# Kernel tuning notes

Measured on AMD Instinct MI355X. Metric: run time of the kernel, lower is better.

Reference implementation:

```python
import jax, jax.numpy as jnp
import numpy as np

EMBED, HEADS, LEVELS, POINTS = 256, 8, 3, 4
SPATIAL = np.array([[128, 128], [64, 64], [32, 32]], dtype=np.int64)  # (H, W) per level
B = 2
S = int((SPATIAL[:, 0] * SPATIAL[:, 1]).sum())  # 21504
Q = S  # encoder self-attention: queries == flattened multi-scale features


def grid_sample_bilinear(img, grid):
    """img: [N,C,H,W]; grid: [N,Q,P,2] (x,y) in [-1,1]; bilinear, zeros padding, align_corners=False.
    Returns [N,C,Q,P]."""
    N, C, H, W = img.shape
    _, Qn, Pn, _ = grid.shape
    x = (grid[..., 0] + 1.0) * (W * 0.5) - 0.5
    y = (grid[..., 1] + 1.0) * (H * 0.5) - 0.5
    x0 = jnp.floor(x)
    y0 = jnp.floor(y)
    wx1 = x - x0
    wy1 = y - y0
    x0i = x0.astype(jnp.int32)
    y0i = y0.astype(jnp.int32)
    imgf = img.reshape(N, C, H * W)

    def gather(ix, iy):
        valid = (ix >= 0) & (ix < W) & (iy >= 0) & (iy < H)
        ixc = jnp.clip(ix, 0, W - 1)
        iyc = jnp.clip(iy, 0, H - 1)
        flat = (iyc * W + ixc).reshape(N, -1)  # [N, Q*P]
        v = jax.vmap(lambda im, f: im[:, f])(imgf, flat)  # [N, C, Q*P]
        return jnp.where(valid.reshape(N, 1, -1), v, 0.0)

    w00 = ((1.0 - wx1) * (1.0 - wy1)).reshape(N, 1, -1)
    w01 = (wx1 * (1.0 - wy1)).reshape(N, 1, -1)
    w10 = ((1.0 - wx1) * wy1).reshape(N, 1, -1)
    w11 = (wx1 * wy1).reshape(N, 1, -1)
    out = (gather(x0i, y0i) * w00 + gather(x0i + 1, y0i) * w01
           + gather(x0i, y0i + 1) * w10 + gather(x0i + 1, y0i + 1) * w11)
    return out.reshape(N, C, Qn, Pn)


def msda_forward(hidden_states, encoder_hidden_states, reference_points, shapes_np,
                 sampling_offsets_w, sampling_offsets_b, attention_weights_w, attention_weights_b,
                 value_proj_w, value_proj_b, output_proj_w, output_proj_b):
    Bn, Qn, E = hidden_states.shape
    H, L, P = HEADS, LEVELS, POINTS
    D = E // H
    Sn = encoder_hidden_states.shape[1]
    value = (encoder_hidden_states @ value_proj_w.T + value_proj_b).reshape(Bn, Sn, H, D)
    off = (hidden_states @ sampling_offsets_w.T + sampling_offsets_b).reshape(Bn, Qn, H, L, P, 2)
    aw = hidden_states @ attention_weights_w.T + attention_weights_b
    aw = jax.nn.softmax(aw.reshape(Bn, Qn, H, L * P), axis=-1).reshape(Bn, Qn, H, L, P)
    # offset normalizer is (W, H) per level
    norm = jnp.asarray(np.stack([shapes_np[:, 1], shapes_np[:, 0]], axis=-1), dtype=hidden_states.dtype)
    loc = reference_points[:, :, None, :, None, :] + off / norm[None, None, None, :, None, :]
    grids = 2.0 * loc - 1.0  # [B,Q,H,L,P,2]
    out = jnp.zeros((Bn * H, D, Qn), value.dtype)
    start = 0
    for lvl in range(L):  # small static loop over levels (distinct spatial shapes)
        h, w = int(shapes_np[lvl, 0]), int(shapes_np[lvl, 1])
        val_l = value[:, start:start + h * w].transpose(0, 2, 3, 1).reshape(Bn * H, D, h, w)
        start += h * w
        g = grids[:, :, :, lvl].transpose(0, 2, 1, 3, 4).reshape(Bn * H, Qn, P, 2)
        sampled = grid_sample_bilinear(val_l, g)  # [B*H, D, Q, P]
        w_l = aw[:, :, :, lvl].transpose(0, 2, 1, 3).reshape(Bn * H, 1, Qn, P)
        out = out + (sampled * w_l).sum(-1)
    out = out.reshape(Bn, H * D, Qn).transpose(0, 2, 1)  # [B,Q,E]
    return out @ output_proj_w.T + output_proj_b


def setup_inputs():
    key = jax.random.key(0)
    ks = jax.random.split(key, 11)
    sc = 0.02
    E, H, L, P = EMBED, HEADS, LEVELS, POINTS
    return {
        "hidden_states": jax.random.normal(ks[0], (B, Q, E), jnp.float32),
        "encoder_hidden_states": jax.random.normal(ks[1], (B, S, E), jnp.float32),
        "reference_points": jax.random.uniform(ks[2], (B, Q, L, 2), jnp.float32),
        "spatial_shapes": jnp.asarray(SPATIAL),
        "sampling_offsets_w": jax.random.normal(ks[3], (H * L * P * 2, E), jnp.float32) * sc,
        "sampling_offsets_b": jax.random.normal(ks[4], (H * L * P * 2,), jnp.float32) * sc,
        "attention_weights_w": jax.random.normal(ks[5], (H * L * P, E), jnp.float32) * sc,
        "attention_weights_b": jax.random.normal(ks[6], (H * L * P,), jnp.float32) * sc,
        "value_proj_w": jax.random.normal(ks[7], (E, E), jnp.float32) * sc,
        "value_proj_b": jax.random.normal(ks[8], (E,), jnp.float32) * sc,
        "output_proj_w": jax.random.normal(ks[9], (E, E), jnp.float32) * sc,
        "output_proj_b": jax.random.normal(ks[10], (E,), jnp.float32) * sc,
    }


def reference(hidden_states, encoder_hidden_states, reference_points, spatial_shapes,
              sampling_offsets_w, sampling_offsets_b, attention_weights_w, attention_weights_b,
              value_proj_w, value_proj_b, output_proj_w, output_proj_b):
    shapes_np = np.asarray(spatial_shapes)  # static per-level (H, W)
    return msda_forward(hidden_states, encoder_hidden_states, reference_points, shapes_np,
                        sampling_offsets_w, sampling_offsets_b, attention_weights_w, attention_weights_b,
                        value_proj_w, value_proj_b, output_proj_w, output_proj_b)
```

## Files before the change

### kernel.cpp

```cpp
#include <hip/hip_runtime.h>
#include <hip/hip_bf16.h>

#define EMBED   256
#define HEADS   8
#define LEVELS  3
#define POINTS  4
#define BATCH   2
#define QLEN    21504
#define SLEN    21504
#define MTOT    (BATCH * QLEN)

typedef __attribute__((ext_vector_type(8))) short short8;
typedef __attribute__((ext_vector_type(4))) float f32x4;

__device__ __forceinline__ short f2bf(float x) {
    unsigned u = __builtin_bit_cast(unsigned, x);
    u += 0x7fffu + ((u >> 16) & 1u);
    return (short)(u >> 16);
}
__device__ __forceinline__ float bf_lo(unsigned u) { return __builtin_bit_cast(float, u << 16); }
__device__ __forceinline__ float bf_hi(unsigned u) { return __builtin_bit_cast(float, u & 0xffff0000u); }
__device__ __forceinline__ void async16(const void* g, void* l) {
    __builtin_amdgcn_global_load_lds((const __attribute__((address_space(1))) void*)g,
                                     (__attribute__((address_space(3))) void*)l, 16, 0, 0);
}

__global__ __launch_bounds__(256)
void pack_weights_kernel(const float* __restrict__ vW, const float* __restrict__ oW,
                         const float* __restrict__ soW, const float* __restrict__ awW,
                         const float* __restrict__ soB, const float* __restrict__ awB,
                         short* __restrict__ vWb, short* __restrict__ oWb,
                         short* __restrict__ soawWb, float* __restrict__ soawB)
{
    int i = blockIdx.x * 256 + threadIdx.x;
    if (i < 65536) {
        vWb[i] = f2bf(vW[i]);
    } else if (i < 131072) {
        int j = i - 65536;
        oWb[j] = f2bf(oW[j]);
    } else if (i < 229376) {
        int j = i - 131072;
        int row = j >> 8, k = j & 255;
        float v = (row < 192) ? soW[row * 256 + k]
                 : (row < 288) ? awW[(row - 192) * 256 + k] : 0.f;
        soawWb[j] = f2bf(v);
    } else if (i < 229760) {
        int row = i - 229376;
        soawB[row] = (row < 192) ? soB[row] : (row < 288) ? awB[row - 192] : 0.f;
    }
}

template<bool A_FP32, bool OUT_BF16>
__device__ __forceinline__
void stream_gemm(const void* __restrict__ Aptr, const short* __restrict__ Wt,
                 const float* __restrict__ bias, void* __restrict__ Cout,
                 int ldc, int colbase, int rowstrip, short* __restrict__ Ws)
{
    const int tid  = threadIdx.x;
    const int lane = tid & 63;
    const int wv   = tid >> 6;
    const int m16  = lane & 15;
    const int ko   = lane >> 4;

    #pragma unroll
    for (int i = 0; i < 16; ++i) {
        const int c    = i * 256 + tid;
        const int colL = c >> 5;
        const int cw   = c & 31;
        const int csw  = (cw & 24) | ((cw ^ colL) & 7);
        async16(Wt + (((size_t)(colbase + colL)) << 8) + csw * 8, Ws + c * 8);
    }

    const int row = rowstrip + wv * 16 + m16;
    short8 afr[8];
    if (A_FP32) {
        const float* Af = (const float*)Aptr + (size_t)row * 256 + ko * 8;
        #pragma unroll
        for (int kt = 0; kt < 8; ++kt) {
            float4 x = *(const float4*)(Af + kt * 32);
            float4 y = *(const float4*)(Af + kt * 32 + 4);
            short8 t;
            t[0] = f2bf(x.x); t[1] = f2bf(x.y); t[2] = f2bf(x.z); t[3] = f2bf(x.w);
            t[4] = f2bf(y.x); t[5] = f2bf(y.y); t[6] = f2bf(y.z); t[7] = f2bf(y.w);
            afr[kt] = t;
        }
    } else {
        const short* Ab = (const short*)Aptr + (size_t)row * 256 + ko * 8;
        #pragma unroll
        for (int kt = 0; kt < 8; ++kt) afr[kt] = *(const short8*)(Ab + kt * 32);
    }

    __syncthreads();

    const short8* Wvp = (const short8*)Ws;
    const int r0 = rowstrip + wv * 16 + ko * 4;
    #pragma unroll
    for (int ct = 0; ct < 8; ++ct) {
        const int colL = ct * 16 + m16;
        const int rowc = colL * 32;
        f32x4 a = (f32x4)0.f;
        #pragma unroll
        for (int kt = 0; kt < 8; ++kt) {
            const int g = kt * 4 + ko;
            const int s = (g & 24) | ((g ^ colL) & 7);
            a = __builtin_amdgcn_mfma_f32_16x16x32_bf16(afr[kt], Wvp[rowc + s], a, 0, 0, 0);
        }
        const int col = colbase + colL;
        const float bv = bias[col];
        #pragma unroll
        for (int r = 0; r < 4; ++r) {
            const float v = a[r] + bv;
            if (OUT_BF16) ((short*)Cout)[(size_t)(r0 + r) * ldc + col] = f2bf(v);
            else          ((float*)Cout)[(size_t)(r0 + r) * ldc + col] = v;
        }
    }
}

__global__ __launch_bounds__(256)
void proj_gemm_kernel(const float* __restrict__ enc, const short* __restrict__ vWb,
                      const float* __restrict__ vB, short* __restrict__ valb,
                      const float* __restrict__ hs, const short* __restrict__ soawWb,
                      const float* __restrict__ soawB, float* __restrict__ offaw)
{
    __shared__ short Ws[128 * 256];
    const int rowstrip = blockIdx.y * 64;
    if (blockIdx.x < 2) {
        stream_gemm<true, true>(enc, vWb, vB, valb, 256, blockIdx.x * 128, rowstrip, Ws);
    } else {
        stream_gemm<true, false>(hs, soawWb, soawB, offaw, 384, (blockIdx.x - 2) * 128, rowstrip, Ws);
    }
}

__global__ __launch_bounds__(256)
void out_gemm_kernel(const short* __restrict__ A, const short* __restrict__ oWb,
                     const float* __restrict__ oB, float* __restrict__ C)
{
    __shared__ short Ws[128 * 256];
    stream_gemm<false, false>(A, oWb, oB, C, 256, blockIdx.x * 128, blockIdx.y * 64, Ws);
}

__global__ __launch_bounds__(256)
void msda_sample_kernel(const short* __restrict__ value,
                        const float* __restrict__ offaw,
                        const float* __restrict__ ref,
                        short* __restrict__ attn)
{
    __shared__ int prep[64 * 100];

    const int tid = threadIdx.x;
    const int g   = tid >> 2;
    const int sub = tid & 3;
    const int lq  = g >> 3;
    const int h   = g & 7;
    const int bq  = blockIdx.x * 8 + lq;
    const int b   = bq / QLEN;

    {
        const float* awp = offaw + (size_t)bq * 384 + 192 + h * 12;
        float w[12];
        #pragma unroll
        for (int i = 0; i < 12; ++i) w[i] = awp[i];
        float mx = w[0];
        #pragma unroll
        for (int i = 1; i < 12; ++i) mx = fmaxf(mx, w[i]);
        float s = 0.f;
        #pragma unroll
        for (int i = 0; i < 12; ++i) s += __expf(w[i] - mx);
        const float inv = 1.f / s;

        const float* offp = offaw + (size_t)bq * 384 + h * 24;
        const float* refp = ref + (size_t)bq * 6;

        #pragma unroll
        for (int it = 0; it < 3; ++it) {
            const int p  = sub + it * 4;
            const int l  = p >> 2;
            const int Wl = 128 >> l;
            const int st = (l == 0) ? 0 : (l == 1 ? 16384 : 20480);

            const float ox = offp[p * 2 + 0];
            const float oy = offp[p * 2 + 1];
            const float rx = refp[2 * l + 0];
            const float ry = refp[2 * l + 1];
            const float a  = __expf(w[p] - mx) * inv;

            const float x = fmaf(rx, (float)Wl, ox - 0.5f);
            const float y = fmaf(ry, (float)Wl, oy - 0.5f);
            const float x0f = floorf(x), y0f = floorf(y);
            const int   x0  = (int)x0f,  y0  = (int)y0f;
            const float wx1 = x - x0f, wy1 = y - y0f;
            const float wx0 = 1.f - wx1, wy0 = 1.f - wy1;
            const bool vx0 = (unsigned)x0       < (unsigned)Wl;
            const bool vx1 = (unsigned)(x0 + 1) < (unsigned)Wl;
            const bool vy0 = (unsigned)y0       < (unsigned)Wl;
            const bool vy1 = (unsigned)(y0 + 1) < (unsigned)Wl;

            const int r0c = (b * SLEN + st + y0 * Wl + x0) * 32 + h * 4;
            int4 idx; float4 wvv;
            idx.x = (vy0 && vx0) ? r0c                : 0;
            idx.y = (vy0 && vx1) ? r0c + 32           : 0;
            idx.z = (vy1 && vx0) ? r0c + Wl * 32      : 0;
            idx.w = (vy1 && vx1) ? r0c + Wl * 32 + 32 : 0;
            wvv.x = (vy0 && vx0) ? wy0 * wx0 * a : 0.f;
            wvv.y = (vy0 && vx1) ? wy0 * wx1 * a : 0.f;
            wvv.z = (vy1 && vx0) ? wy1 * wx0 * a : 0.f;
            wvv.w = (vy1 && vx1) ? wy1 * wx1 * a : 0.f;

            *(int4*)  &prep[g * 100 + p * 8]     = idx;
            *(float4*)&prep[g * 100 + p * 8 + 4] = wvv;
        }
    }
    __syncthreads();

    const int4* vp = (const int4*)value;
    float acc[8];
    #pragma unroll
    for (int j = 0; j < 8; ++j) acc[j] = 0.f;

    #pragma unroll
    for (int p = 0; p < 12; ++p) {
        const int4   idx = *(const int4*)  &prep[g * 100 + p * 8];
        const float4 wvv = *(const float4*)&prep[g * 100 + p * 8 + 4];
        const int4 v0 = vp[idx.x + sub];
        const int4 v1 = vp[idx.y + sub];
        const int4 v2 = vp[idx.z + sub];
        const int4 v3 = vp[idx.w + sub];
        #define ACCUM(V, W) \
            acc[0] = fmaf(W, bf_lo((unsigned)V.x), acc[0]); \
            acc[1] = fmaf(W, bf_hi((unsigned)V.x), acc[1]); \
            acc[2] = fmaf(W, bf_lo((unsigned)V.y), acc[2]); \
            acc[3] = fmaf(W, bf_hi((unsigned)V.y), acc[3]); \
            acc[4] = fmaf(W, bf_lo((unsigned)V.z), acc[4]); \
            acc[5] = fmaf(W, bf_hi((unsigned)V.z), acc[5]); \
            acc[6] = fmaf(W, bf_lo((unsigned)V.w), acc[6]); \
            acc[7] = fmaf(W, bf_hi((unsigned)V.w), acc[7]);
        ACCUM(v0, wvv.x) ACCUM(v1, wvv.y) ACCUM(v2, wvv.z) ACCUM(v3, wvv.w)
        #undef ACCUM
    }

    int4 o;
    o.x = ((unsigned)(unsigned short)f2bf(acc[1]) << 16) | (unsigned short)f2bf(acc[0]);
    o.y = ((unsigned)(unsigned short)f2bf(acc[3]) << 16) | (unsigned short)f2bf(acc[2]);
    o.z = ((unsigned)(unsigned short)f2bf(acc[5]) << 16) | (unsigned short)f2bf(acc[4]);
    o.w = ((unsigned)(unsigned short)f2bf(acc[7]) << 16) | (unsigned short)f2bf(acc[6]);
    ((int4*)attn)[(size_t)bq * 32 + h * 4 + sub] = o;
}

extern "C" void kernel_launch(void* const* d_in, const int* in_sizes, int n_in,
                              void* d_out, int out_size, void* d_ws, size_t ws_size,
                              hipStream_t stream) {
    const float* hs  = (const float*)d_in[0];
    const float* enc = (const float*)d_in[1];
    const float* rp  = (const float*)d_in[2];
    const float* soW = (const float*)d_in[4];
    const float* soB = (const float*)d_in[5];
    const float* awW = (const float*)d_in[6];
    const float* awB = (const float*)d_in[7];
    const float* vW  = (const float*)d_in[8];
    const float* vB  = (const float*)d_in[9];
    const float* oW  = (const float*)d_in[10];
    const float* oB  = (const float*)d_in[11];
    float* out = (float*)d_out;

    const int M = MTOT;
    const size_t ME = (size_t)M * 256;

    short* valb   = (short*)d_ws;
    short* attnb  = valb + ME;
    float* offaw  = (float*)(attnb + ME);
    short* vWb    = (short*)(offaw + (size_t)M * 384);
    short* oWb    = vWb + 65536;
    short* soawWb = oWb + 65536;
    float* soawB  = (float*)(soawWb + 98304);

    dim3 blk(256);
    pack_weights_kernel<<<dim3(898), blk, 0, stream>>>(vW, oW, soW, awW, soB, awB,
                                                       vWb, oWb, soawWb, soawB);
    proj_gemm_kernel<<<dim3(5, M / 64), blk, 0, stream>>>(enc, vWb, vB, valb,
                                                          hs, soawWb, soawB, offaw);
    msda_sample_kernel<<<dim3(M / 8), blk, 0, stream>>>(valb, offaw, rp, attnb);
    out_gemm_kernel<<<dim3(2, M / 64), blk, 0, stream>>>(attnb, oWb, oB, out);
}
```

Before: 266.2 us.

## Restructure GEMMs with A-stationary tiles and head-major value layout for sampling

The projection and output GEMMs now keep the A fragments in registers and loop over weight column groups inside one 512-thread block with 128-row strips, instead of launching a block per column tile. The offset/attention-weight output drops its zero padding from 384 to 288 columns. Values are stored head-major ([b,h,s,32]) so that horizontally adjacent texels are contiguous. The sampler clamps x into a two-texel window so each bilinear point needs two row loads split across 8 lanes, with partial sums combined by a shuffle. The aim is to cut redundant A reloads, padded GEMM work and gather count, at the cost of strided scatter stores for value and more lanes per query.

```diff
diff --git a/kernel.cpp b/kernel.cpp
--- a/kernel.cpp
+++ b/kernel.cpp
@@ -38,105 +38,120 @@
     } else if (i < 131072) {
         int j = i - 65536;
         oWb[j] = f2bf(oW[j]);
-    } else if (i < 229376) {
+    } else if (i < 204800) {
         int j = i - 131072;
         int row = j >> 8, k = j & 255;
-        float v = (row < 192) ? soW[row * 256 + k]
-                 : (row < 288) ? awW[(row - 192) * 256 + k] : 0.f;
+        float v = (row < 192) ? soW[row * 256 + k] : awW[(row - 192) * 256 + k];
         soawWb[j] = f2bf(v);
-    } else if (i < 229760) {
-        int row = i - 229376;
-        soawB[row] = (row < 192) ? soB[row] : (row < 288) ? awB[row - 192] : 0.f;
-    }
-}
-
-template<bool A_FP32, bool OUT_BF16>
+    } else if (i < 205088) {
+        int row = i - 204800;
+        soawB[row] = (row < 192) ? soB[row] : awB[row - 192];
+    }
+}
+
 __device__ __forceinline__
-void stream_gemm(const void* __restrict__ Aptr, const short* __restrict__ Wt,
-                 const float* __restrict__ bias, void* __restrict__ Cout,
-                 int ldc, int colbase, int rowstrip, short* __restrict__ Ws)
+void astat_gemm(const short8* __restrict__ afr, const short* __restrict__ Wt,
+                const float* __restrict__ bias, int ngroups, int gcols,
+                int rowstrip, short* __restrict__ Ws,
+                int mode, int ldc, void* __restrict__ Cout)
 {
     const int tid  = threadIdx.x;
     const int lane = tid & 63;
     const int wv   = tid >> 6;
     const int m16  = lane & 15;
     const int ko   = lane >> 4;
-
-    #pragma unroll
-    for (int i = 0; i < 16; ++i) {
-        const int c    = i * 256 + tid;
-        const int colL = c >> 5;
-        const int cw   = c & 31;
-        const int csw  = (cw & 24) | ((cw ^ colL) & 7);
-        async16(Wt + (((size_t)(colbase + colL)) << 8) + csw * 8, Ws + c * 8);
-    }
-
-    const int row = rowstrip + wv * 16 + m16;
-    short8 afr[8];
-    if (A_FP32) {
-        const float* Af = (const float*)Aptr + (size_t)row * 256 + ko * 8;
-        #pragma unroll
-        for (int kt = 0; kt < 8; ++kt) {
-            float4 x = *(const float4*)(Af + kt * 32);
-            float4 y = *(const float4*)(Af + kt * 32 + 4);
-            short8 t;
-            t[0] = f2bf(x.x); t[1] = f2bf(x.y); t[2] = f2bf(x.z); t[3] = f2bf(x.w);
-            t[4] = f2bf(y.x); t[5] = f2bf(y.y); t[6] = f2bf(y.z); t[7] = f2bf(y.w);
-            afr[kt] = t;
+    const int nch  = gcols * 32;
+    const int r0   = rowstrip + wv * 16 + ko * 4;
+
+    for (int gidx = 0; gidx < ngroups; ++gidx) {
+        const int colbase = gidx * gcols;
+        for (int c = tid; c < nch; c += 512) {
+            const int colL = c >> 5;
+            const int cw   = c & 31;
+            const int csw  = (cw & 24) | ((cw ^ colL) & 7);
+            async16(Wt + (((size_t)(colbase + colL)) << 8) + csw * 8, Ws + c * 8);
         }
-    } else {
-        const short* Ab = (const short*)Aptr + (size_t)row * 256 + ko * 8;
-        #pragma unroll
-        for (int kt = 0; kt < 8; ++kt) afr[kt] = *(const short8*)(Ab + kt * 32);
-    }
-
-    __syncthreads();
-
-    const short8* Wvp = (const short8*)Ws;
-    const int r0 = rowstrip + wv * 16 + ko * 4;
-    #pragma unroll
-    for (int ct = 0; ct < 8; ++ct) {
-        const int colL = ct * 16 + m16;
-        const int rowc = colL * 32;
-        f32x4 a = (f32x4)0.f;
-        #pragma unroll
-        for (int kt = 0; kt < 8; ++kt) {
-            const int g = kt * 4 + ko;
-            const int s = (g & 24) | ((g ^ colL) & 7);
-            a = __builtin_amdgcn_mfma_f32_16x16x32_bf16(afr[kt], Wvp[rowc + s], a, 0, 0, 0);
+        __syncthreads();
+        const short8* Wvp = (const short8*)Ws;
+        const int nct = gcols >> 4;
+        for (int ct = 0; ct < nct; ++ct) {
+            const int colL = ct * 16 + m16;
+            f32x4 a = (f32x4)0.f;
+            #pragma unroll
+            for (int kt = 0; kt < 8; ++kt) {
+                const int g = kt * 4 + ko;
+                const int s = (g & 24) | ((g ^ colL) & 7);
+                a = __builtin_amdgcn_mfma_f32_16x16x32_bf16(afr[kt], Wvp[colL * 32 + s], a, 0, 0, 0);
+            }
+            const int col = colbase + colL;
+            const float bv = bias[col];
+            if (mode == 1) {
+                const int h = col >> 5, ch = col & 31;
+                #pragma unroll
+                for (int r = 0; r < 4; ++r) {
+                    const int rg = r0 + r;
+                    const int b  = (rg >= SLEN) ? 1 : 0;
+                    const int sx = rg - b * SLEN;
+                    ((short*)Cout)[(((size_t)(b * 8 + h)) * SLEN + sx) * 32 + ch] = f2bf(a[r] + bv);
+                }
+            } else {
+                #pragma unroll
+                for (int r = 0; r < 4; ++r)
+                    ((float*)Cout)[(size_t)(r0 + r) * ldc + col] = a[r] + bv;
+            }
         }
-        const int col = colbase + colL;
-        const float bv = bias[col];
-        #pragma unroll
-        for (int r = 0; r < 4; ++r) {
-            const float v = a[r] + bv;
-            if (OUT_BF16) ((short*)Cout)[(size_t)(r0 + r) * ldc + col] = f2bf(v);
-            else          ((float*)Cout)[(size_t)(r0 + r) * ldc + col] = v;
-        }
-    }
-}
-
-__global__ __launch_bounds__(256)
+        __syncthreads();
+    }
+}
+
+__global__ __launch_bounds__(512)
 void proj_gemm_kernel(const float* __restrict__ enc, const short* __restrict__ vWb,
                       const float* __restrict__ vB, short* __restrict__ valb,
                       const float* __restrict__ hs, const short* __restrict__ soawWb,
                       const float* __restrict__ soawB, float* __restrict__ offaw)
 {
     __shared__ short Ws[128 * 256];
-    const int rowstrip = blockIdx.y * 64;
-    if (blockIdx.x < 2) {
-        stream_gemm<true, true>(enc, vWb, vB, valb, 256, blockIdx.x * 128, rowstrip, Ws);
-    } else {
-        stream_gemm<true, false>(hs, soawWb, soawB, offaw, 384, (blockIdx.x - 2) * 128, rowstrip, Ws);
-    }
-}
-
-__global__ __launch_bounds__(256)
+    const int tid = threadIdx.x;
+    const int lane = tid & 63, wv = tid >> 6;
+    const int m16 = lane & 15, ko = lane >> 4;
+    const int rowstrip = blockIdx.y * 128;
+    const bool isVal = (blockIdx.x == 0);
+    const float* A = isVal ? enc : hs;
+    const int row = rowstrip + wv * 16 + m16;
+
+    short8 afr[8];
+    const float* Af = A + (size_t)row * 256 + ko * 8;
+    #pragma unroll
+    for (int kt = 0; kt < 8; ++kt) {
+        float4 x = *(const float4*)(Af + kt * 32);
+        float4 y = *(const float4*)(Af + kt * 32 + 4);
+        short8 t;
+        t[0] = f2bf(x.x); t[1] = f2bf(x.y); t[2] = f2bf(x.z); t[3] = f2bf(x.w);
+        t[4] = f2bf(y.x); t[5] = f2bf(y.y); t[6] = f2bf(y.z); t[7] = f2bf(y.w);
+        afr[kt] = t;
+    }
+
+    if (isVal) astat_gemm(afr, vWb,    vB,    2, 128, rowstrip, Ws, 1, 256, valb);
+    else       astat_gemm(afr, soawWb, soawB, 3,  96, rowstrip, Ws, 0, 288, offaw);
+}
+
+__global__ __launch_bounds__(512)
 void out_gemm_kernel(const short* __restrict__ A, const short* __restrict__ oWb,
                      const float* __restrict__ oB, float* __restrict__ C)
 {
     __shared__ short Ws[128 * 256];
-    stream_gemm<false, false>(A, oWb, oB, C, 256, blockIdx.x * 128, blockIdx.y * 64, Ws);
+    const int tid = threadIdx.x;
+    const int lane = tid & 63, wv = tid >> 6;
+    const int m16 = lane & 15, ko = lane >> 4;
+    const int rowstrip = blockIdx.x * 128;
+    const int row = rowstrip + wv * 16 + m16;
+
+    short8 afr[8];
+    const short* Ab = A + (size_t)row * 256 + ko * 8;
+    #pragma unroll
+    for (int kt = 0; kt < 8; ++kt) afr[kt] = *(const short8*)(Ab + kt * 32);
+
+    astat_gemm(afr, oWb, oB, 2, 128, rowstrip, Ws, 0, 256, C);
 }
 
 __global__ __launch_bounds__(256)
@@ -145,18 +160,19 @@
                         const float* __restrict__ ref,
                         short* __restrict__ attn)
 {
-    __shared__ int prep[64 * 100];
+    __shared__ int prep[32 * 76];
 
     const int tid = threadIdx.x;
-    const int g   = tid >> 2;
-    const int sub = tid & 3;
+    const int g   = tid >> 3;
+    const int sub = tid & 7;
+    const int t   = sub >> 2;
     const int lq  = g >> 3;
     const int h   = g & 7;
-    const int bq  = blockIdx.x * 8 + lq;
-    const int b   = bq / QLEN;
+    const int bq  = blockIdx.x * 4 + lq;
+    const int b   = (bq >= QLEN) ? 1 : 0;
 
     {
-        const float* awp = offaw + (size_t)bq * 384 + 192 + h * 12;
+        const float* awp = offaw + (size_t)bq * 288 + 192 + h * 12;
         float w[12];
         #pragma unroll
         for (int i = 0; i < 12; ++i) w[i] = awp[i];
@@ -168,12 +184,13 @@
         for (int i = 0; i < 12; ++i) s += __expf(w[i] - mx);
         const float inv = 1.f / s;
 
-        const float* offp = offaw + (size_t)bq * 384 + h * 24;
+        const float* offp = offaw + (size_t)bq * 288 + h * 24;
         const float* refp = ref + (size_t)bq * 6;
-
+        const int npts = (sub < 4) ? 2 : 1;
         #pragma unroll
-        for (int it = 0; it < 3; ++it) {
-            const int p  = sub + it * 4;
+        for (int it = 0; it < 2; ++it) {
+            if (it >= npts) break;
+            const int p  = sub + it * 8;
             const int l  = p >> 2;
             const int Wl = 128 >> l;
             const int st = (l == 0) ? 0 : (l == 1 ? 16384 : 20480);
@@ -190,24 +207,24 @@
             const int   x0  = (int)x0f,  y0  = (int)y0f;
             const float wx1 = x - x0f, wy1 = y - y0f;
             const float wx0 = 1.f - wx1, wy0 = 1.f - wy1;
-            const bool vx0 = (unsigned)x0       < (unsigned)Wl;
-            const bool vx1 = (unsigned)(x0 + 1) < (unsigned)Wl;
             const bool vy0 = (unsigned)y0       < (unsigned)Wl;
             const bool vy1 = (unsigned)(y0 + 1) < (unsigned)Wl;
 
-            const int r0c = (b * SLEN + st + y0 * Wl + x0) * 32 + h * 4;
-            int4 idx; float4 wvv;
-            idx.x = (vy0 && vx0) ? r0c                : 0;
-            idx.y = (vy0 && vx1) ? r0c + 32           : 0;
-            idx.z = (vy1 && vx0) ? r0c + Wl * 32      : 0;
-            idx.w = (vy1 && vx1) ? r0c + Wl * 32 + 32 : 0;
-            wvv.x = (vy0 && vx0) ? wy0 * wx0 * a : 0.f;
-            wvv.y = (vy0 && vx1) ? wy0 * wx1 * a : 0.f;
-            wvv.z = (vy1 && vx0) ? wy1 * wx0 * a : 0.f;
-            wvv.w = (vy1 && vx1) ? wy1 * wx1 * a : 0.f;
-
-            *(int4*)  &prep[g * 100 + p * 8]     = idx;
-            *(float4*)&prep[g * 100 + p * 8 + 4] = wvv;
+            const int xs = min(max(x0, 0), Wl - 2);
+            const float wl0 = (xs == x0) ? wx0 : ((xs == x0 + 1) ? wx1 : 0.f);
+            const float wl1 = (xs == x0) ? wx1 : ((xs + 1 == x0) ? wx0 : 0.f);
+
+            const int hb = (b * 8 + h) * SLEN + st;
+            const int i0 = vy0 ? (hb + y0 * Wl + xs) * 4       : 0;
+            const int i1 = vy1 ? (hb + (y0 + 1) * Wl + xs) * 4 : 0;
+
+            int* pp = &prep[g * 76 + p * 6];
+            pp[0] = i0;
+            pp[1] = i1;
+            pp[2] = __builtin_bit_cast(int, vy0 ? wy0 * wl0 * a : 0.f);
+            pp[3] = __builtin_bit_cast(int, vy0 ? wy0 * wl1 * a : 0.f);
+            pp[4] = __builtin_bit_cast(int, vy1 ? wy1 * wl0 * a : 0.f);
+            pp[5] = __builtin_bit_cast(int, vy1 ? wy1 * wl1 * a : 0.f);
         }
     }
     __syncthreads();
@@ -219,12 +236,13 @@
 
     #pragma unroll
     for (int p = 0; p < 12; ++p) {
-        const int4   idx = *(const int4*)  &prep[g * 100 + p * 8];
-        const float4 wvv = *(const float4*)&prep[g * 100 + p * 8 + 4];
-        const int4 v0 = vp[idx.x + sub];
-        const int4 v1 = vp[idx.y + sub];
-        const int4 v2 = vp[idx.z + sub];
-        const int4 v3 = vp[idx.w + sub];
+        const int* pp = &prep[g * 76 + p * 6];
+        const int i0 = pp[0];
+        const int i1 = pp[1];
+        const float w0 = __builtin_bit_cast(float, pp[2 + t]);
+        const float w1 = __builtin_bit_cast(float, pp[4 + t]);
+        const int4 v0 = vp[i0 + sub];
+        const int4 v1 = vp[i1 + sub];
         #define ACCUM(V, W) \
             acc[0] = fmaf(W, bf_lo((unsigned)V.x), acc[0]); \
             acc[1] = fmaf(W, bf_hi((unsigned)V.x), acc[1]); \
@@ -234,16 +252,21 @@
             acc[5] = fmaf(W, bf_hi((unsigned)V.z), acc[5]); \
             acc[6] = fmaf(W, bf_lo((unsigned)V.w), acc[6]); \
             acc[7] = fmaf(W, bf_hi((unsigned)V.w), acc[7]);
-        ACCUM(v0, wvv.x) ACCUM(v1, wvv.y) ACCUM(v2, wvv.z) ACCUM(v3, wvv.w)
+        ACCUM(v0, w0) ACCUM(v1, w1)
         #undef ACCUM
     }
 
-    int4 o;
-    o.x = ((unsigned)(unsigned short)f2bf(acc[1]) << 16) | (unsigned short)f2bf(acc[0]);
-    o.y = ((unsigned)(unsigned short)f2bf(acc[3]) << 16) | (unsigned short)f2bf(acc[2]);
-    o.z = ((unsigned)(unsigned short)f2bf(acc[5]) << 16) | (unsigned short)f2bf(acc[4]);
-    o.w = ((unsigned)(unsigned short)f2bf(acc[7]) << 16) | (unsigned short)f2bf(acc[6]);
-    ((int4*)attn)[(size_t)bq * 32 + h * 4 + sub] = o;
+    #pragma unroll
+    for (int j = 0; j < 8; ++j) acc[j] += __shfl_xor(acc[j], 4);
+
+    if (sub < 4) {
+        int4 o;
+        o.x = ((unsigned)(unsigned short)f2bf(acc[1]) << 16) | (unsigned short)f2bf(acc[0]);
+        o.y = ((unsigned)(unsigned short)f2bf(acc[3]) << 16) | (unsigned short)f2bf(acc[2]);
+        o.z = ((unsigned)(unsigned short)f2bf(acc[5]) << 16) | (unsigned short)f2bf(acc[4]);
+        o.w = ((unsigned)(unsigned short)f2bf(acc[7]) << 16) | (unsigned short)f2bf(acc[6]);
+        ((int4*)attn)[(size_t)bq * 32 + h * 4 + sub] = o;
+    }
 }
 
 extern "C" void kernel_launch(void* const* d_in, const int* in_sizes, int n_in,
@@ -268,16 +291,15 @@
     short* valb   = (short*)d_ws;
     short* attnb  = valb + ME;
     float* offaw  = (float*)(attnb + ME);
-    short* vWb    = (short*)(offaw + (size_t)M * 384);
+    short* vWb    = (short*)(offaw + (size_t)M * 288);
     short* oWb    = vWb + 65536;
     short* soawWb = oWb + 65536;
-    float* soawB  = (float*)(soawWb + 98304);
-
-    dim3 blk(256);
-    pack_weights_kernel<<<dim3(898), blk, 0, stream>>>(vW, oW, soW, awW, soB, awB,
-                                                       vWb, oWb, soawWb, soawB);
-    proj_gemm_kernel<<<dim3(5, M / 64), blk, 0, stream>>>(enc, vWb, vB, valb,
-                                                          hs, soawWb, soawB, offaw);
-    msda_sample_kernel<<<dim3(M / 8), blk, 0, stream>>>(valb, offaw, rp, attnb);
-    out_gemm_kernel<<<dim3(2, M / 64), blk, 0, stream>>>(attnb, oWb, oB, out);
-}
+    float* soawB  = (float*)(soawWb + 73728);
+
+    pack_weights_kernel<<<dim3(802), dim3(256), 0, stream>>>(vW, oW, soW, awW, soB, awB,
+                                                             vWb, oWb, soawWb, soawB);
+    proj_gemm_kernel<<<dim3(2, M / 128), dim3(512), 0, stream>>>(enc, vWb, vB, valb,
+                                                                 hs, soawWb, soawB, offaw);
+    msda_sample_kernel<<<dim3(M / 4), dim3(256), 0, stream>>>(valb, offaw, rp, attnb);
+    out_gemm_kernel<<<dim3(M / 128), dim3(512), 0, stream>>>(attnb, oWb, oB, out);
+}
```

Result: faster. 244.6 us (-8.1%).
